# Optimization experiments

Hardware: AMD Instinct MI355X
Metric: run time of the kernel (lower is better)

## Reference

```python
import jax, jax.numpy as jnp
import numpy as np

DIM = 1024
N_HEADS = 16
HEAD_DIM = DIM // N_HEADS


def setup_inputs() -> dict:
    key = jax.random.key(0)
    ks = jax.random.split(key, 5)
    x = jax.random.normal(ks[0], (2, 2048, DIM), dtype=jnp.float32)
    # nn.Linear-style init scale
    s = 1.0 / np.sqrt(DIM)
    W_qkv = jax.random.uniform(ks[1], (DIM, 3 * DIM), jnp.float32, -s, s)
    b_qkv = jax.random.uniform(ks[2], (3 * DIM,), jnp.float32, -s, s)
    W_proj = jax.random.uniform(ks[3], (DIM, DIM), jnp.float32, -s, s)
    b_proj = jax.random.uniform(ks[4], (DIM,), jnp.float32, -s, s)
    return {"x": x, "W_qkv": W_qkv, "b_qkv": b_qkv, "W_proj": W_proj, "b_proj": b_proj}


def reference(x, W_qkv, b_qkv, W_proj, b_proj):
    B, S, D = x.shape
    scale = HEAD_DIM ** -0.5
    qkv = x @ W_qkv + b_qkv                                   # [B,S,3D]
    qkv = qkv.reshape(B, S, 3, N_HEADS, HEAD_DIM)
    q = qkv[:, :, 0].transpose(0, 2, 1, 3)                    # [B,H,S,d]
    k = qkv[:, :, 1].transpose(0, 2, 1, 3)
    v = qkv[:, :, 2].transpose(0, 2, 1, 3)
    attn = jnp.einsum('bhqd,bhkd->bhqk', q, k) * scale        # [B,H,S,S]
    attn = jax.nn.softmax(attn, axis=-1)
    out = jnp.einsum('bhqk,bhkd->bhqd', attn, v)              # [B,H,S,d]
    out = out.transpose(0, 2, 1, 3).reshape(B, S, D)
    return out @ W_proj + b_proj
```

## Files before the change

kernel.cpp:

```cpp
#include <hip/hip_runtime.h>
#include <stdint.h>

typedef unsigned short u16;
typedef __attribute__((ext_vector_type(8))) short bf16x8;
typedef __attribute__((ext_vector_type(4))) float f32x4;
typedef __attribute__((ext_vector_type(16))) float f32x16;
typedef __attribute__((ext_vector_type(4))) u16 us4;
typedef __attribute__((ext_vector_type(8))) u16 us8;

__device__ __forceinline__ u16 f2bf(float f) {
  union { float f; unsigned u; } v; v.f = f;
  unsigned r = v.u + 0x7fffu + ((v.u >> 16) & 1u);
  return (u16)(r >> 16);
}

__device__ __forceinline__ float bf2f(u16 b) {
  union { float f; unsigned u; } v; v.u = ((unsigned)b) << 16;
  return v.f;
}

__device__ __forceinline__ unsigned pkbf(float a, float b) {
  union { float f; unsigned u; } x, y; x.f = a; y.f = b;
  return __builtin_amdgcn_perm(y.u + 0x8000u, x.u + 0x8000u, 0x07060302u);
}

__device__ __forceinline__ float fast_exp2(float x) {
#if __has_builtin(__builtin_amdgcn_exp2f)
  return __builtin_amdgcn_exp2f(x);
#else
  return exp2f(x);
#endif
}

__device__ __forceinline__ void gld16(const void* g, void* l) {
  __builtin_amdgcn_global_load_lds(
      (const __attribute__((address_space(1))) void*)g,
      (__attribute__((address_space(3))) void*)l, 16, 0, 0);
}

__global__ void cvt_kernel(const float* __restrict__ in, u16* __restrict__ out, int n4) {
  int i = blockIdx.x * blockDim.x + threadIdx.x;
  if (i >= n4) return;
  f32x4 v = ((const f32x4*)in)[i];
  us4 r;
#pragma unroll
  for (int j = 0; j < 4; ++j) r[j] = f2bf(v[j]);
  ((us4*)out)[i] = r;
}

__global__ void transw_kernel(const float* __restrict__ in, u16* __restrict__ out, int R, int C) {
  __shared__ u16 tile[32][33];
  const int tx = threadIdx.x & 31, ty = threadIdx.x >> 5;
  const int c0 = blockIdx.x * 32, r0 = blockIdx.y * 32;
#pragma unroll
  for (int j = 0; j < 4; ++j)
    tile[ty + j * 8][tx] = f2bf(in[(size_t)(r0 + ty + j * 8) * C + c0 + tx]);
  __syncthreads();
#pragma unroll
  for (int j = 0; j < 4; ++j)
    out[(size_t)(c0 + ty + j * 8) * R + r0 + tx] = tile[tx][ty + j * 8];
}

__global__ __launch_bounds__(256) void qkv_gemm_kernel(
    const u16* __restrict__ A, const u16* __restrict__ Bt, const float* __restrict__ bias,
    u16* __restrict__ Qb, u16* __restrict__ Kb, u16* __restrict__ Vtb) {
  __shared__ u16 sm[17408];
  u16* As = sm;
  u16* Bs = sm + 4096;
  const int tid = threadIdx.x;
  const int w = tid >> 6, l = tid & 63, quad = l >> 4, lanelo = l & 15;
  const int wr = w >> 1, wc = w & 1;
  const int flat = blockIdx.x + 32 * blockIdx.y;
  const int xcd = flat & 7, lid = flat >> 3;
  const long m0 = (long)((xcd >> 1) * 8 + (lid & 7)) * 128;
  const long n0 = (long)((xcd & 1) * 12 + (lid >> 3)) * 128;

  f32x4 acc[4][4];
#pragma unroll
  for (int i = 0; i < 4; ++i)
#pragma unroll
    for (int j = 0; j < 4; ++j) acc[i][j] = (f32x4){0.f, 0.f, 0.f, 0.f};

  const u16* ag = A + (m0 + w * 32 + (l >> 2)) * 1024 + (l & 3) * 8;
  const u16* bg = Bt + (n0 + w * 32 + (l >> 2)) * 1024 + (l & 3) * 8;
  u16* asl = As + w * 1024;
  u16* bsl = Bs + w * 1024;

  for (int kt = 0; kt < 32; ++kt) {
    const int ko = kt * 32;
    gld16(ag + ko, asl);
    gld16(ag + 16 * 1024 + ko, asl + 512);
    gld16(bg + ko, bsl);
    gld16(bg + 16 * 1024 + ko, bsl + 512);
    __syncthreads();
    bf16x8 af[4], bf[4];
#pragma unroll
    for (int mt = 0; mt < 4; ++mt)
      af[mt] = *(const bf16x8*)(As + (wr * 64 + mt * 16 + lanelo) * 32 + quad * 8);
#pragma unroll
    for (int nt = 0; nt < 4; ++nt)
      bf[nt] = *(const bf16x8*)(Bs + (wc * 64 + nt * 16 + lanelo) * 32 + quad * 8);
#pragma unroll
    for (int mt = 0; mt < 4; ++mt)
#pragma unroll
      for (int nt = 0; nt < 4; ++nt)
        acc[mt][nt] = __builtin_amdgcn_mfma_f32_16x16x32_bf16(af[mt], bf[nt], acc[mt][nt], 0, 0, 0);
    __syncthreads();
  }

  const int t = (int)(n0 >> 10);
  const float scl = (t == 0) ? 0.18033688011112042f : 1.0f;

  float bias_v[4];
#pragma unroll
  for (int nt = 0; nt < 4; ++nt) bias_v[nt] = bias[n0 + wc * 64 + nt * 16 + lanelo];

  u16* Ct = sm;
#pragma unroll
  for (int mt = 0; mt < 4; ++mt)
#pragma unroll
    for (int nt = 0; nt < 4; ++nt)
#pragma unroll
      for (int r = 0; r < 4; ++r)
        Ct[(wr * 64 + mt * 16 + quad * 4 + r) * 136 + wc * 64 + nt * 16 + lanelo] =
            f2bf((acc[mt][nt][r] + bias_v[nt]) * scl);
  __syncthreads();

  const int b = (int)(m0 >> 11);
  const int s0 = (int)(m0 & 2047);
  const int h0 = (int)((n0 & 1023) >> 6);

  if (t < 2) {
    u16* dst = (t == 0) ? Qb : Kb;
#pragma unroll
    for (int p = 0; p < 8; ++p) {
      const int hh = p >> 2;
      const int sl = (p & 3) * 32 + (tid >> 3);
      const int c8 = tid & 7;
      us8 v = *(const us8*)(Ct + sl * 136 + hh * 64 + c8 * 8);
      const int pos = (c8 + sl) & 7;
      const size_t off = ((size_t)((b * 16 + h0 + hh) * 2048 + s0 + sl)) * 64 + pos * 8;
      *(us8*)(dst + off) = v;
    }
  } else {
#pragma unroll
    for (int p = 0; p < 8; ++p) {
      const int hh = p >> 2;
      const int dl = (p & 3) * 16 + (tid >> 4);
      const int c16 = tid & 15;
      us8 v;
#pragma unroll
      for (int j = 0; j < 8; ++j) v[j] = Ct[(c16 * 8 + j) * 136 + hh * 64 + dl];
      const int pos = (c16 + dl) & 15;
      const size_t off = ((size_t)((b * 16 + h0 + hh) * 64 + dl)) * 2048 + s0 + pos * 8;
      *(us8*)(Vtb + off) = v;
    }
  }
}

__global__ __launch_bounds__(256, 4) void attn_kernel(
    const u16* __restrict__ Qb, const u16* __restrict__ Kb,
    const u16* __restrict__ Vtb, u16* __restrict__ Op, float* __restrict__ lp) {
  __shared__ u16 Ks[8192];
  __shared__ u16 Vs[8192];
  const int tid = threadIdx.x;
  const int w = tid >> 6, l = tid & 63;
  const int m = l & 31, hi = l >> 5;
  const int qt = blockIdx.x, head = blockIdx.y, z = blockIdx.z;
  const u16* Qh = Qb + (size_t)head * 2048 * 64;
  const u16* Kh = Kb + (size_t)head * 2048 * 64;
  const u16* Vh = Vtb + (size_t)head * 64 * 2048;
  const int permaddr = (l ^ 32) << 2;

  const int qrow = qt * 128 + w * 32 + m;
  bf16x8 qf[4];
#pragma unroll
  for (int ks = 0; ks < 4; ++ks) {
    const int c = ks * 2 + hi;
    const int pos = (c + qrow) & 7;
    qf[ks] = *(const bf16x8*)(Qh + (size_t)qrow * 64 + pos * 8);
  }

  f32x16 o0, o1, os32;
#pragma unroll
  for (int i = 0; i < 16; ++i) { o0[i] = 0.f; o1[i] = 0.f; os32[i] = 0.f; }
  bf16x8 ones;
#pragma unroll
  for (int j = 0; j < 8; ++j) ones[j] = (short)0x3F80;

  for (int kt = 0; kt < 8; ++kt) {
    const int kb = z * 8 + kt;
    const u16* kbase = Kh + (size_t)kb * 8192;
#pragma unroll
    for (int j = 0; j < 4; ++j) {
      const int i = w * 4 + j;
      gld16(kbase + i * 512 + l * 8, &Ks[i * 512]);
    }
#pragma unroll
    for (int j = 0; j < 4; ++j) {
      const int i = w * 4 + j;
      const int dd = i * 4 + (l >> 4);
      gld16(Vh + (size_t)dd * 2048 + kb * 128 + (l & 15) * 8, &Vs[i * 512]);
    }
    __syncthreads();

#pragma unroll
    for (int g = 0; g < 4; ++g) {
      f32x16 st;
#pragma unroll
      for (int i = 0; i < 16; ++i) st[i] = 0.f;
      const int key = g * 32 + m;
#pragma unroll
      for (int ks = 0; ks < 4; ++ks) {
        const int c = ks * 2 + hi;
        const int pos = (c + key) & 7;
        bf16x8 kf = *(const bf16x8*)(&Ks[key * 64 + pos * 8]);
        st = __builtin_amdgcn_mfma_f32_32x32x16_bf16(kf, qf[ks], st, 0, 0, 0);
      }

      float p[16];
#pragma unroll
      for (int r = 0; r < 16; ++r) p[r] = fast_exp2(st[r]);

      unsigned L[8];
#pragma unroll
      for (int q4 = 0; q4 < 4; ++q4) {
        L[2 * q4] = pkbf(p[4 * q4], p[4 * q4 + 1]);
        L[2 * q4 + 1] = pkbf(p[4 * q4 + 2], p[4 * q4 + 3]);
      }

#pragma unroll
      for (int s = 0; s < 2; ++s) {
        const unsigned a0 = L[4 * s], a1 = L[4 * s + 1];
        const unsigned b0 = L[4 * s + 2], b1 = L[4 * s + 3];
        const unsigned s0 = hi ? a0 : b0;
        const unsigned s1 = hi ? a1 : b1;
        const unsigned r0 = (unsigned)__builtin_amdgcn_ds_bpermute(permaddr, (int)s0);
        const unsigned r1 = (unsigned)__builtin_amdgcn_ds_bpermute(permaddr, (int)s1);
        int4 fd;
        fd.x = (int)(hi ? r0 : a0);
        fd.y = (int)(hi ? r1 : a1);
        fd.z = (int)(hi ? b0 : r0);
        fd.w = (int)(hi ? b1 : r1);
        union { int4 i; bf16x8 v; } pu; pu.i = fd;
        os32 = __builtin_amdgcn_mfma_f32_32x32x16_bf16(pu.v, ones, os32, 0, 0, 0);
        const int c = g * 4 + s * 2 + hi;
#pragma unroll
        for (int n = 0; n < 2; ++n) {
          const int d = n * 32 + m;
          const int pos = (c + d) & 15;
          bf16x8 vf = *(const bf16x8*)(&Vs[d * 128 + pos * 8]);
          if (n == 0) o0 = __builtin_amdgcn_mfma_f32_32x32x16_bf16(pu.v, vf, o0, 0, 0, 0);
          else        o1 = __builtin_amdgcn_mfma_f32_32x32x16_bf16(pu.v, vf, o1, 0, 0, 0);
        }
      }
    }
    __syncthreads();
  }

  if (m == 0) {
#pragma unroll
    for (int r = 0; r < 16; ++r) {
      const int q = (r & 3) + 8 * (r >> 2) + 4 * hi;
      lp[(size_t)z * 65536 + (size_t)head * 2048 + qt * 128 + w * 32 + q] = os32[r];
    }
  }

  const int b = head >> 4, h = head & 15;
  u16* Od = Op + (size_t)z * 4194304;
#pragma unroll
  for (int r = 0; r < 16; ++r) {
    const int qlocal = (r & 3) + 8 * (r >> 2) + 4 * hi;
    const size_t base =
        ((size_t)(b * 2048 + qt * 128 + w * 32 + qlocal)) * 1024 + h * 64;
    Od[base + m] = f2bf(o0[r]);
    Od[base + 32 + m] = f2bf(o1[r]);
  }
}

__global__ __launch_bounds__(128) void combine_kernel(
    const u16* __restrict__ Op, const float* __restrict__ lp, u16* __restrict__ Ob) {
  const int r = blockIdx.x;
  const int tid = threadIdx.x;
  const int col = tid * 8;
  const int b = r >> 11, s = r & 2047, h = col >> 6;
  const size_t li = (size_t)(b * 16 + h) * 2048 + s;
  const float linv = 1.0f / (lp[li] + lp[65536 + li]);
  us8 v0 = *(const us8*)(Op + (size_t)r * 1024 + col);
  us8 v1 = *(const us8*)(Op + 4194304 + (size_t)r * 1024 + col);
  us8 o;
#pragma unroll
  for (int j = 0; j < 8; ++j)
    o[j] = f2bf((bf2f(v0[j]) + bf2f(v1[j])) * linv);
  *(us8*)(Ob + (size_t)r * 1024 + col) = o;
}

__global__ __launch_bounds__(256) void proj_gemm_kernel(
    const u16* __restrict__ A, const u16* __restrict__ Bt,
    const float* __restrict__ bias, float* __restrict__ out) {
  __shared__ u16 sm[6144];
  u16* As = sm;
  u16* Bs = sm + 4096;
  const int tid = threadIdx.x;
  const int w = tid >> 6, l = tid & 63, quad = l >> 4, lanelo = l & 15;
  const int wr = w >> 1, wc = w & 1;
  const int flat = blockIdx.x + 32 * blockIdx.y;
  const int xcd = flat & 7, lid = flat >> 3;
  const long m0 = (long)(xcd * 4 + (lid & 3)) * 128;
  const long n0 = (long)(lid >> 2) * 64;

  f32x4 acc[4][2];
#pragma unroll
  for (int i = 0; i < 4; ++i)
#pragma unroll
    for (int j = 0; j < 2; ++j) acc[i][j] = (f32x4){0.f, 0.f, 0.f, 0.f};

  const u16* ag = A + (m0 + w * 32 + (l >> 2)) * 1024 + (l & 3) * 8;
  const u16* bg = Bt + (n0 + w * 16 + (l >> 2)) * 1024 + (l & 3) * 8;
  u16* asl = As + w * 1024;
  u16* bsl = Bs + w * 512;

  for (int kt = 0; kt < 32; ++kt) {
    const int ko = kt * 32;
    gld16(ag + ko, asl);
    gld16(ag + 16 * 1024 + ko, asl + 512);
    gld16(bg + ko, bsl);
    __syncthreads();
    bf16x8 af[4], bf[2];
#pragma unroll
    for (int mt = 0; mt < 4; ++mt)
      af[mt] = *(const bf16x8*)(As + (wr * 64 + mt * 16 + lanelo) * 32 + quad * 8);
#pragma unroll
    for (int nt = 0; nt < 2; ++nt)
      bf[nt] = *(const bf16x8*)(Bs + (wc * 32 + nt * 16 + lanelo) * 32 + quad * 8);
#pragma unroll
    for (int mt = 0; mt < 4; ++mt)
#pragma unroll
      for (int nt = 0; nt < 2; ++nt)
        acc[mt][nt] = __builtin_amdgcn_mfma_f32_16x16x32_bf16(af[mt], bf[nt], acc[mt][nt], 0, 0, 0);
    __syncthreads();
  }

  float bias_v[2];
#pragma unroll
  for (int nt = 0; nt < 2; ++nt)
    bias_v[nt] = bias[n0 + wc * 32 + nt * 16 + lanelo];

#pragma unroll
  for (int mt = 0; mt < 4; ++mt)
#pragma unroll
    for (int nt = 0; nt < 2; ++nt)
#pragma unroll
      for (int r = 0; r < 4; ++r) {
        const size_t mm = m0 + wr * 64 + mt * 16 + quad * 4 + r;
        const size_t nn = n0 + wc * 32 + nt * 16 + lanelo;
        out[mm * 1024 + nn] = acc[mt][nt][r] + bias_v[nt];
      }
}

extern "C" void kernel_launch(void* const* d_in, const int* in_sizes, int n_in,
                              void* d_out, int out_size, void* d_ws, size_t ws_size,
                              hipStream_t stream) {
  const float* x = (const float*)d_in[0];
  const float* Wqkv = (const float*)d_in[1];
  const float* bqkv = (const float*)d_in[2];
  const float* Wproj = (const float*)d_in[3];
  const float* bproj = (const float*)d_in[4];
  float* out = (float*)d_out;
  char* ws = (char*)d_ws;

  u16* Xb   = (u16*)(ws);
  u16* Op   = (u16*)(ws);
  u16* Wqkt = (u16*)(ws + 8388608);
  u16* Qb   = (u16*)(ws + 16777216);
  u16* Ob   = (u16*)(ws + 16777216);
  u16* Kb   = (u16*)(ws + 25165824);
  u16* Vtb  = (u16*)(ws + 33554432);
  u16* Wpt  = (u16*)(ws + 41943040);
  float* lp = (float*)(ws + 44040192);

  cvt_kernel<<<4096, 256, 0, stream>>>(x, Xb, 1048576);
  transw_kernel<<<dim3(96, 32), 256, 0, stream>>>(Wqkv, Wqkt, 1024, 3072);
  transw_kernel<<<dim3(32, 32), 256, 0, stream>>>(Wproj, Wpt, 1024, 1024);
  qkv_gemm_kernel<<<dim3(32, 24), 256, 0, stream>>>(Xb, Wqkt, bqkv, Qb, Kb, Vtb);
  attn_kernel<<<dim3(16, 32, 2), 256, 0, stream>>>(Qb, Kb, Vtb, Op, lp);
  combine_kernel<<<4096, 128, 0, stream>>>(Op, lp, Ob);
  proj_gemm_kernel<<<dim3(32, 16), 256, 0, stream>>>(Ob, Wpt, bproj, out);
}
```

Measured before the change: 193.5 us.

## Fuse prep kernels, remap attention grid, compute row sums with VALU

The three conversion and transpose kernels are merged into one prep kernel launch, removing two launches. The attention grid becomes a flat 1D index that remaps head, query tile and split so that co-scheduled blocks are grouped differently. The softmax denominator is now summed in scalar registers plus one cross-half bpermute, replacing the extra MFMA against a ones vector and freeing 16 accumulator registers. The trade-off is extra VALU adds per tile and a more branchy prep kernel.

```diff
diff --git a/kernel.cpp b/kernel.cpp
--- a/kernel.cpp
+++ b/kernel.cpp
@@ -38,20 +38,29 @@
       (__attribute__((address_space(3))) void*)l, 16, 0, 0);
 }
 
-__global__ void cvt_kernel(const float* __restrict__ in, u16* __restrict__ out, int n4) {
-  int i = blockIdx.x * blockDim.x + threadIdx.x;
-  if (i >= n4) return;
-  f32x4 v = ((const f32x4*)in)[i];
-  us4 r;
-#pragma unroll
-  for (int j = 0; j < 4; ++j) r[j] = f2bf(v[j]);
-  ((us4*)out)[i] = r;
-}
-
-__global__ void transw_kernel(const float* __restrict__ in, u16* __restrict__ out, int R, int C) {
+__global__ void prep_kernel(const float* __restrict__ x, u16* __restrict__ Xb,
+                            const float* __restrict__ Wqkv, u16* __restrict__ Wqkt,
+                            const float* __restrict__ Wproj, u16* __restrict__ Wpt) {
   __shared__ u16 tile[32][33];
+  const int blk = blockIdx.x;
+  if (blk < 4096) {
+    const int i = blk * 256 + threadIdx.x;
+    f32x4 v = ((const f32x4*)x)[i];
+    us4 r;
+#pragma unroll
+    for (int j = 0; j < 4; ++j) r[j] = f2bf(v[j]);
+    ((us4*)Xb)[i] = r;
+    return;
+  }
+  const float* in;
+  u16* out;
+  int R, C, t;
+  if (blk < 7168) { in = Wqkv; out = Wqkt; R = 1024; C = 3072; t = blk - 4096; }
+  else            { in = Wproj; out = Wpt; R = 1024; C = 1024; t = blk - 7168; }
+  const int gx = (C == 3072) ? (t % 96) : (t % 32);
+  const int gy = (C == 3072) ? (t / 96) : (t / 32);
   const int tx = threadIdx.x & 31, ty = threadIdx.x >> 5;
-  const int c0 = blockIdx.x * 32, r0 = blockIdx.y * 32;
+  const int c0 = gx * 32, r0 = gy * 32;
 #pragma unroll
   for (int j = 0; j < 4; ++j)
     tile[ty + j * 8][tx] = f2bf(in[(size_t)(r0 + ty + j * 8) * C + c0 + tx]);
@@ -166,7 +175,10 @@
   const int tid = threadIdx.x;
   const int w = tid >> 6, l = tid & 63;
   const int m = l & 31, hi = l >> 5;
-  const int qt = blockIdx.x, head = blockIdx.y, z = blockIdx.z;
+  const int fid = blockIdx.x;
+  const int head = (fid & 7) + 8 * ((fid >> 3) & 3);
+  const int qt = (fid >> 5) & 15;
+  const int z = fid >> 9;
   const u16* Qh = Qb + (size_t)head * 2048 * 64;
   const u16* Kh = Kb + (size_t)head * 2048 * 64;
   const u16* Vh = Vtb + (size_t)head * 64 * 2048;
@@ -181,12 +193,10 @@
     qf[ks] = *(const bf16x8*)(Qh + (size_t)qrow * 64 + pos * 8);
   }
 
-  f32x16 o0, o1, os32;
-#pragma unroll
-  for (int i = 0; i < 16; ++i) { o0[i] = 0.f; o1[i] = 0.f; os32[i] = 0.f; }
-  bf16x8 ones;
-#pragma unroll
-  for (int j = 0; j < 8; ++j) ones[j] = (short)0x3F80;
+  f32x16 o0, o1;
+#pragma unroll
+  for (int i = 0; i < 16; ++i) { o0[i] = 0.f; o1[i] = 0.f; }
+  float sacc = 0.f;
 
   for (int kt = 0; kt < 8; ++kt) {
     const int kb = z * 8 + kt;
@@ -221,6 +231,8 @@
       float p[16];
 #pragma unroll
       for (int r = 0; r < 16; ++r) p[r] = fast_exp2(st[r]);
+#pragma unroll
+      for (int r = 0; r < 16; ++r) sacc += p[r];
 
       unsigned L[8];
 #pragma unroll
@@ -243,7 +255,6 @@
         fd.z = (int)(hi ? b0 : r0);
         fd.w = (int)(hi ? b1 : r1);
         union { int4 i; bf16x8 v; } pu; pu.i = fd;
-        os32 = __builtin_amdgcn_mfma_f32_32x32x16_bf16(pu.v, ones, os32, 0, 0, 0);
         const int c = g * 4 + s * 2 + hi;
 #pragma unroll
         for (int n = 0; n < 2; ++n) {
@@ -258,13 +269,11 @@
     __syncthreads();
   }
 
-  if (m == 0) {
-#pragma unroll
-    for (int r = 0; r < 16; ++r) {
-      const int q = (r & 3) + 8 * (r >> 2) + 4 * hi;
-      lp[(size_t)z * 65536 + (size_t)head * 2048 + qt * 128 + w * 32 + q] = os32[r];
-    }
-  }
+  union { float f; int i; } sv; sv.f = sacc;
+  union { float f; int i; } pv; pv.i = __builtin_amdgcn_ds_bpermute(permaddr, sv.i);
+  const float ltot = sacc + pv.f;
+  if (hi == 0)
+    lp[(size_t)z * 65536 + (size_t)head * 2048 + qt * 128 + w * 32 + m] = ltot;
 
   const int b = head >> 4, h = head & 15;
   u16* Od = Op + (size_t)z * 4194304;
@@ -379,11 +388,9 @@
   u16* Wpt  = (u16*)(ws + 41943040);
   float* lp = (float*)(ws + 44040192);
 
-  cvt_kernel<<<4096, 256, 0, stream>>>(x, Xb, 1048576);
-  transw_kernel<<<dim3(96, 32), 256, 0, stream>>>(Wqkv, Wqkt, 1024, 3072);
-  transw_kernel<<<dim3(32, 32), 256, 0, stream>>>(Wproj, Wpt, 1024, 1024);
+  prep_kernel<<<8192, 256, 0, stream>>>(x, Xb, Wqkv, Wqkt, Wproj, Wpt);
   qkv_gemm_kernel<<<dim3(32, 24), 256, 0, stream>>>(Xb, Wqkt, bqkv, Qb, Kb, Vtb);
-  attn_kernel<<<dim3(16, 32, 2), 256, 0, stream>>>(Qb, Kb, Vtb, Op, lp);
+  attn_kernel<<<1024, 256, 0, stream>>>(Qb, Kb, Vtb, Op, lp);
   combine_kernel<<<4096, 128, 0, stream>>>(Op, lp, Ob);
   proj_gemm_kernel<<<dim3(32, 16), 256, 0, stream>>>(Ob, Wpt, bproj, out);
 }
```

After: 188.4 us. 2.7% less time.
